# Kernel optimization log

Measured on AMD Instinct MI355X. Metric: run time of the kernel, lower is better.

The kernel has to match this reference:

```python
import jax, jax.numpy as jnp
import numpy as np
import math

FILT = 5
CENTER = FILT / 2 - 0.5          # filtSide/2 - 0.5 from calculate_weights
LN_E = math.log(2.71828)         # real(2.71828**(i*t)) == cos(t*ln(2.71828))
CUTOFF = math.sqrt(CENTER * CENTER + 0.25)
OUT_CH, IN_CH = 16, 8


def _zernike_tables(out_ch, in_ch):
    """Replicates the (n, m) index walk and the polys() coefficients."""
    K = out_ch * in_ch
    n, m = 2, 0
    ns, ms = [], []
    for _ in range(K):
        if m == n:
            n += 1
            m = 0
        else:
            m += 1
        ns.append(n)
        ms.append(m)
    S = max(1, max((nn - mm) // 2 for nn, mm in zip(ns, ms)))
    C = np.zeros((K, S), np.float64)   # top/bot coefficient per (pair, s)
    E = np.zeros((K, S), np.int32)     # exponent n - 2s per (pair, s)
    for p, (nn, mm) in enumerate(zip(ns, ms)):
        for s in range((nn - mm) // 2):
            top = (-1) ** s * math.factorial(nn - s)
            bot = (math.factorial(s)
                   * math.gamma((nn + mm) / 2 - s + 1)
                   * math.gamma((nn - mm) / 2 - s) + 1)
            C[p, s] = top / bot
            E[p, s] = nn - 2 * s
    return C.astype(np.float32), E, np.array(ns, np.int32)


def setup_inputs() -> dict:
    key = jax.random.key(0)
    B, H, W = 8, 1024, 1024
    x = jax.random.normal(key, (B, IN_CH, H, W), dtype=jnp.float32)
    C, E, N = _zernike_tables(OUT_CH, IN_CH)
    return {
        "x": x,
        "coeff": jnp.asarray(C),           # [K, S] float32
        "expn": jnp.asarray(E),            # [K, S] int32
        "nvals": jnp.asarray(N),           # [K]    int32
    }


def _zernike_weights(coeff, expn, nvals):
    # kernel grid geometry (radialDist)
    ii = jnp.arange(FILT, dtype=jnp.float32)[:, None]
    jj = jnp.arange(FILT, dtype=jnp.float32)[None, :]
    a = jnp.abs(ii - CENTER)
    b = jnp.abs(jj - CENTER)
    dist = jnp.sqrt(a * a + b * b)
    radial = jnp.where(dist <= CUTOFF, dist, 0.0)          # [5,5]
    rsafe = jnp.where(radial > 0, radial, 1.0)             # avoid 0**0 / grad NaNs
    # polys: poly[p,i,j] = sum_s C[p,s] * r^(n-2s), only where radial>0
    terms = coeff[:, :, None, None] * rsafe[None, None] ** expn[:, :, None, None].astype(jnp.float32)
    poly = jnp.where(radial > 0, jnp.sum(terms, axis=1), 0.0)   # [K,5,5]
    # expo: multiply by real(2.71828**(i*n*phi)) only where poly>0
    phi = jnp.arctan(b / (a + 0.001))                      # [5,5]
    cosr = jnp.cos(nvals[:, None, None].astype(jnp.float32) * phi * LN_E)
    w = jnp.where(poly > 0, poly * cosr, poly)
    return w.reshape(OUT_CH, IN_CH, FILT, FILT)


def reference(x, coeff, expn, nvals):
    w = _zernike_weights(coeff, expn, nvals)
    return jax.lax.conv_general_dilated(
        x, w,
        window_strides=(1, 1),
        padding=((2, 2), (2, 2)),
        dimension_numbers=("NCHW", "OIHW", "NCHW"),
    )
```

## Files before the change

kernel.cpp:

```cpp
#include <hip/hip_runtime.h>


typedef __attribute__((ext_vector_type(8))) short bf16x8;
typedef __attribute__((ext_vector_type(4))) float f32x4;

#define OUT_CH 16
#define IN_CH  8
#define FILT   5
#define NTAPS  28
#define IMG    1024
#define TH     16
#define TW     64
#define LR     (TH + 4)
#define LC     (TW + 4)

static __device__ __forceinline__ unsigned short f32_to_bf16_rne(float f) {
    unsigned int u = __float_as_uint(f);
    u = u + 0x7fffu + ((u >> 16) & 1u);
    return (unsigned short)(u >> 16);
}
static __device__ __forceinline__ float bf16_bits_to_f32(unsigned short h) {
    return __uint_as_float(((unsigned int)h) << 16);
}

__global__ void zernike_weights_kernel(const float* __restrict__ coeff,
                                       const int* __restrict__ expn,
                                       const int* __restrict__ nvals,
                                       int K, int S,
                                       unsigned short* __restrict__ whi,
                                       unsigned short* __restrict__ wlo) {
    int p = threadIdx.x;
    if (p >= K) return;
    const float CENTER = 2.0f;
    const float CUTOFF = sqrtf(4.25f);
    const float LNE    = 0.99999932734f;
    int co = p >> 3, ci = p & 7;
    float nv = (float)nvals[p];

    for (int tap = 0; tap < NTAPS; ++tap) {
        float w = 0.0f;
        if (tap < 25) {
            int i = tap / 5, j = tap % 5;
            float a = fabsf((float)i - CENTER);
            float b = fabsf((float)j - CENTER);
            float dist = sqrtf(a * a + b * b);
            float radial = (dist <= CUTOFF) ? dist : 0.0f;
            float rsafe = (radial > 0.0f) ? radial : 1.0f;
            float poly = 0.0f;
            for (int s = 0; s < S; ++s) {
                float C = coeff[p * S + s];
                int   e = expn[p * S + s];
                float pw = 1.0f;
                for (int t = 0; t < e; ++t) pw *= rsafe;
                poly += C * pw;
            }
            if (!(radial > 0.0f)) poly = 0.0f;
            float phi  = atanf(b / (a + 0.001f));
            float cosr = cosf(nv * phi * LNE);
            w = (poly > 0.0f) ? poly * cosr : poly;
        }
        unsigned short hi = f32_to_bf16_rne(w);
        unsigned short lo = f32_to_bf16_rne(w - bf16_bits_to_f32(hi));
        int idx = (co * NTAPS + tap) * 8 + ci;
        whi[idx] = hi;
        wlo[idx] = lo;
    }
}

__global__ __launch_bounds__(256) void conv_mfma_kernel(
        const float* __restrict__ x,
        const unsigned short* __restrict__ whi,
        const unsigned short* __restrict__ wlo,
        float* __restrict__ out) {
    __shared__ uint4 tile[LR * LC];

    const int tx   = blockIdx.x * TW;
    const int ty   = blockIdx.y * TH;
    const int b    = blockIdx.z;
    const int tid  = threadIdx.x;
    const int lane = tid & 63;
    const int wv   = tid >> 6;
    const int quad = lane >> 4;
    const int n15  = lane & 15;

    bf16x8 a_hi[7], a_lo[7];
#pragma unroll
    for (int q = 0; q < 7; ++q) {
        int tap = q * 4 + quad;
        int off = (n15 * NTAPS + tap) * 8;
        a_hi[q] = *(const bf16x8*)(whi + off);
        a_lo[q] = *(const bf16x8*)(wlo + off);
    }

    for (int pix = tid; pix < LR * LC; pix += 256) {
        int r = pix / LC, c = pix - r * LC;
        int gy = ty + r - 2;
        int gx = tx + c - 2;
        bool inb = (gy >= 0) & (gy < IMG) & (gx >= 0) & (gx < IMG);
        uint4 u;
        unsigned int pk[4];
#pragma unroll
        for (int ci = 0; ci < 8; ++ci) {
            float v = 0.0f;
            if (inb) v = x[(((b * IN_CH + ci) << 10) + gy << 10) + gx];
            unsigned short h = f32_to_bf16_rne(v);
            if (ci & 1) pk[ci >> 1] |= ((unsigned int)h) << 16;
            else        pk[ci >> 1]  = h;
        }
        u.x = pk[0]; u.y = pk[1]; u.z = pk[2]; u.w = pk[3];
        tile[pix] = u;
    }
    __syncthreads();

    int offq[7];
#pragma unroll
    for (int q = 0; q < 7; ++q) {
        int tap = q * 4 + quad;
        int kh = (tap < 25) ? (tap / 5) : 0;
        int kw = (tap < 25) ? (tap % 5) : 0;
        offq[q] = kh * LC + kw;
    }

    const int row0 = wv * 4;
#pragma unroll
    for (int gr = 0; gr < 4; ++gr) {
        int row = row0 + gr;
#pragma unroll
        for (int gc = 0; gc < 4; ++gc) {
            int c0   = gc * 16;
            int base = row * LC + c0 + n15;
            f32x4 acc_h = {0.f, 0.f, 0.f, 0.f};
            f32x4 acc_l = {0.f, 0.f, 0.f, 0.f};
#pragma unroll
            for (int q = 0; q < 7; ++q) {
                bf16x8 bfrag = *(const bf16x8*)&tile[base + offq[q]];
                acc_h = __builtin_amdgcn_mfma_f32_16x16x32_bf16(a_hi[q], bfrag, acc_h, 0, 0, 0);
                acc_l = __builtin_amdgcn_mfma_f32_16x16x32_bf16(a_lo[q], bfrag, acc_l, 0, 0, 0);
            }
            int gy  = ty + row;
            int gxp = tx + c0 + n15;
#pragma unroll
            for (int r = 0; r < 4; ++r) {
                int co = quad * 4 + r;
                out[(((b * OUT_CH + co) << 10) + gy << 10) + gxp] = acc_h[r] + acc_l[r];
            }
        }
    }
}

extern "C" void kernel_launch(void* const* d_in, const int* in_sizes, int n_in,
                              void* d_out, int out_size, void* d_ws, size_t ws_size,
                              hipStream_t stream) {
    const float* x     = (const float*)d_in[0];
    const float* coeff = (const float*)d_in[1];
    const int*   expn  = (const int*)d_in[2];
    const int*   nvals = (const int*)d_in[3];
    int K = in_sizes[3];
    int S = in_sizes[1] / K;

    unsigned short* whi = (unsigned short*)d_ws;
    unsigned short* wlo = whi + OUT_CH * NTAPS * 8;

    zernike_weights_kernel<<<1, 128, 0, stream>>>(coeff, expn, nvals, K, S, whi, wlo);

    dim3 grid(IMG / TW, IMG / TH, 8);
    conv_mfma_kernel<<<grid, 256, 0, stream>>>(x, whi, wlo, (float*)d_out);
}
```

Baseline: 900.4 us.

## Vectorize halo tile loads with float4 groups and parallelize weight generation per tap

The shared-memory tile fill now loads four consecutive pixels per channel as a float4 instead of scalar loads. The tile is widened to 72 columns so groups are aligned, and the tap offsets shift by 2 to compensate. This cuts the number of global load instructions and the integer index math in the staging loop, at the cost of a slightly larger tile and some redundant halo loads. The weight-generation kernel now spreads its work across one thread per (pair, tap) instead of looping over the taps serially in 128 threads.

Result: faster. 806.2 us (-10.5%).

```diff
diff --git a/kernel.cpp b/kernel.cpp
--- a/kernel.cpp
+++ b/kernel.cpp
@@ -12,7 +12,8 @@
 #define TH     16
 #define TW     64
 #define LR     (TH + 4)
-#define LC     (TW + 4)
+#define LC     72
+#define CGRP   (LC / 4)
 
 static __device__ __forceinline__ unsigned short f32_to_bf16_rne(float f) {
     unsigned int u = __float_as_uint(f);
@@ -22,6 +23,10 @@
 static __device__ __forceinline__ float bf16_bits_to_f32(unsigned short h) {
     return __uint_as_float(((unsigned int)h) << 16);
 }
+static __device__ __forceinline__ unsigned int pk2(float lo, float hi) {
+    return (unsigned int)f32_to_bf16_rne(lo) |
+           ((unsigned int)f32_to_bf16_rne(hi) << 16);
+}
 
 __global__ void zernike_weights_kernel(const float* __restrict__ coeff,
                                        const int* __restrict__ expn,
@@ -29,42 +34,42 @@
                                        int K, int S,
                                        unsigned short* __restrict__ whi,
                                        unsigned short* __restrict__ wlo) {
-    int p = threadIdx.x;
-    if (p >= K) return;
+    int idx = blockIdx.x * blockDim.x + threadIdx.x;
+    if (idx >= K * NTAPS) return;
+    int p   = idx / NTAPS;
+    int tap = idx - p * NTAPS;
     const float CENTER = 2.0f;
     const float CUTOFF = sqrtf(4.25f);
     const float LNE    = 0.99999932734f;
     int co = p >> 3, ci = p & 7;
     float nv = (float)nvals[p];
 
-    for (int tap = 0; tap < NTAPS; ++tap) {
-        float w = 0.0f;
-        if (tap < 25) {
-            int i = tap / 5, j = tap % 5;
-            float a = fabsf((float)i - CENTER);
-            float b = fabsf((float)j - CENTER);
-            float dist = sqrtf(a * a + b * b);
-            float radial = (dist <= CUTOFF) ? dist : 0.0f;
-            float rsafe = (radial > 0.0f) ? radial : 1.0f;
-            float poly = 0.0f;
-            for (int s = 0; s < S; ++s) {
-                float C = coeff[p * S + s];
-                int   e = expn[p * S + s];
-                float pw = 1.0f;
-                for (int t = 0; t < e; ++t) pw *= rsafe;
-                poly += C * pw;
-            }
-            if (!(radial > 0.0f)) poly = 0.0f;
-            float phi  = atanf(b / (a + 0.001f));
-            float cosr = cosf(nv * phi * LNE);
-            w = (poly > 0.0f) ? poly * cosr : poly;
+    float w = 0.0f;
+    if (tap < 25) {
+        int i = tap / 5, j = tap % 5;
+        float a = fabsf((float)i - CENTER);
+        float b = fabsf((float)j - CENTER);
+        float dist = sqrtf(a * a + b * b);
+        float radial = (dist <= CUTOFF) ? dist : 0.0f;
+        float rsafe = (radial > 0.0f) ? radial : 1.0f;
+        float poly = 0.0f;
+        for (int s = 0; s < S; ++s) {
+            float C = coeff[p * S + s];
+            int   e = expn[p * S + s];
+            float pw = 1.0f;
+            for (int t = 0; t < e; ++t) pw *= rsafe;
+            poly += C * pw;
         }
-        unsigned short hi = f32_to_bf16_rne(w);
-        unsigned short lo = f32_to_bf16_rne(w - bf16_bits_to_f32(hi));
-        int idx = (co * NTAPS + tap) * 8 + ci;
-        whi[idx] = hi;
-        wlo[idx] = lo;
+        if (!(radial > 0.0f)) poly = 0.0f;
+        float phi  = atanf(b / (a + 0.001f));
+        float cosr = cosf(nv * phi * LNE);
+        w = (poly > 0.0f) ? poly * cosr : poly;
     }
+    unsigned short hi = f32_to_bf16_rne(w);
+    unsigned short lo = f32_to_bf16_rne(w - bf16_bits_to_f32(hi));
+    int oidx = (co * NTAPS + tap) * 8 + ci;
+    whi[oidx] = hi;
+    wlo[oidx] = lo;
 }
 
 __global__ __launch_bounds__(256) void conv_mfma_kernel(
@@ -92,23 +97,35 @@
         a_lo[q] = *(const bf16x8*)(wlo + off);
     }
 
-    for (int pix = tid; pix < LR * LC; pix += 256) {
-        int r = pix / LC, c = pix - r * LC;
-        int gy = ty + r - 2;
-        int gx = tx + c - 2;
-        bool inb = (gy >= 0) & (gy < IMG) & (gx >= 0) & (gx < IMG);
-        uint4 u;
-        unsigned int pk[4];
+    const float* xb = x + (((long)b * IN_CH) << 20);
+    for (int g = tid; g < LR * CGRP; g += 256) {
+        int r   = g / CGRP;
+        int cg  = g - r * CGRP;
+        int gy  = ty + r - 2;
+        int gx0 = tx + (cg << 2) - 4;
+        uint4 u[4];
+        if (((unsigned)gy < IMG) & ((unsigned)gx0 < IMG)) {
+            const float* px = xb + (gy << 10) + gx0;
+            f32x4 v[8];
 #pragma unroll
-        for (int ci = 0; ci < 8; ++ci) {
-            float v = 0.0f;
-            if (inb) v = x[(((b * IN_CH + ci) << 10) + gy << 10) + gx];
-            unsigned short h = f32_to_bf16_rne(v);
-            if (ci & 1) pk[ci >> 1] |= ((unsigned int)h) << 16;
-            else        pk[ci >> 1]  = h;
+            for (int ci = 0; ci < 8; ++ci)
+                v[ci] = *(const f32x4*)(px + (ci << 20));
+#pragma unroll
+            for (int j = 0; j < 4; ++j) {
+                u[j].x = pk2(v[0][j], v[1][j]);
+                u[j].y = pk2(v[2][j], v[3][j]);
+                u[j].z = pk2(v[4][j], v[5][j]);
+                u[j].w = pk2(v[6][j], v[7][j]);
+            }
+        } else {
+#pragma unroll
+            for (int j = 0; j < 4; ++j) {
+                u[j].x = 0u; u[j].y = 0u; u[j].z = 0u; u[j].w = 0u;
+            }
         }
-        u.x = pk[0]; u.y = pk[1]; u.z = pk[2]; u.w = pk[3];
-        tile[pix] = u;
+        int t0 = r * LC + (cg << 2);
+#pragma unroll
+        for (int j = 0; j < 4; ++j) tile[t0 + j] = u[j];
     }
     __syncthreads();
 
@@ -118,7 +135,7 @@
         int tap = q * 4 + quad;
         int kh = (tap < 25) ? (tap / 5) : 0;
         int kw = (tap < 25) ? (tap % 5) : 0;
-        offq[q] = kh * LC + kw;
+        offq[q] = kh * LC + kw + 2;
     }
 
     const int row0 = wv * 4;
@@ -161,7 +178,9 @@
     unsigned short* whi = (unsigned short*)d_ws;
     unsigned short* wlo = whi + OUT_CH * NTAPS * 8;
 
-    zernike_weights_kernel<<<1, 128, 0, stream>>>(coeff, expn, nvals, K, S, whi, wlo);
+    int wthreads = K * NTAPS;
+    zernike_weights_kernel<<<(wthreads + 255) / 256, 256, 0, stream>>>(
+        coeff, expn, nvals, K, S, whi, wlo);
 
     dim3 grid(IMG / TW, IMG / TH, 8);
     conv_mfma_kernel<<<grid, 256, 0, stream>>>(x, whi, wlo, (float*)d_out);
```
